# Kernel tuning notes

Hardware: AMD Instinct MI355X
Metric: run time of the kernel (lower is better)

Reference implementation:

```python
import jax, jax.numpy as jnp
import numpy as np

N_NODES = 98304
N_GRAPHS = 2048
NODES_PER_GRAPH = 48
N_EDGES = 393216
NODE_IN = 128
EMB = 64
HID = 256
N_LAYERS = 6
ATTN_DIM = 256
N_HEADS = 4
HEAD_DIM = ATTN_DIM // N_HEADS
OUT_DIM = 1024


def setup_inputs() -> dict:
    key = jax.random.key(0)
    ks = iter(jax.random.split(key, 40))

    def nrm(shape, fan_in):
        return (jax.random.normal(next(ks), shape, dtype=jnp.float32)
                / np.float32(np.sqrt(fan_in)))

    x = jax.random.normal(next(ks), (N_NODES, NODE_IN), dtype=jnp.float32)
    edge_index = jax.random.randint(next(ks), (2, N_EDGES), 0, N_NODES, dtype=jnp.int32)
    batch = (jnp.arange(N_NODES, dtype=jnp.int32) // NODES_PER_GRAPH)

    inp = {
        "x": x,
        "edge_index": edge_index,
        "batch": batch,
        "W_embed": nrm((NODE_IN, EMB), NODE_IN),
        "b_embed": jnp.zeros((EMB,), jnp.float32),
        "W1": nrm((N_LAYERS, EMB, HID), EMB),
        "b1": jnp.zeros((N_LAYERS, HID), jnp.float32),
        "W2": nrm((N_LAYERS, HID, 2 * HID), HID),
        "b2": jnp.zeros((N_LAYERS, 2 * HID), jnp.float32),
        "W3": nrm((N_LAYERS, 2 * HID, EMB), 2 * HID),
        "b3": jnp.zeros((N_LAYERS, EMB), jnp.float32),
        "Wp": nrm((EMB, ATTN_DIM), EMB),
        "bp": jnp.zeros((ATTN_DIM,), jnp.float32),
        "q": jax.random.normal(next(ks), (1, ATTN_DIM), dtype=jnp.float32),
        "W_in": nrm((ATTN_DIM, 3 * ATTN_DIM), ATTN_DIM),
        "b_in": jnp.zeros((3 * ATTN_DIM,), jnp.float32),
        "W_out": nrm((ATTN_DIM, ATTN_DIM), ATTN_DIM),
        "b_out": jnp.zeros((ATTN_DIM,), jnp.float32),
        "Wh1": nrm((ATTN_DIM, HID), ATTN_DIM),
        "bh1": jnp.zeros((HID,), jnp.float32),
        "ln_g": jnp.ones((HID,), jnp.float32),
        "ln_b": jnp.zeros((HID,), jnp.float32),
        "Wh2": nrm((HID, OUT_DIM), HID),
        "bh2": jnp.zeros((OUT_DIM,), jnp.float32),
    }
    return inp


def _forward(x, edge_index, batch, W_embed, b_embed, W1, b1, W2, b2, W3, b3,
             Wp, bp, q, W_in, b_in, W_out, b_out, Wh1, bh1, ln_g, ln_b, Wh2, bh2):
    row = edge_index[0]  # only row is used, matching the torch module

    # node embed
    h = x @ W_embed + b_embed  # [N, 64]

    # 6 GNN layers: gather h[row] -> 3-layer MLP -> scatter_add back to row
    for l in range(N_LAYERS):
        m = jax.nn.relu(h[row] @ W1[l] + b1[l])          # [E, 256]
        m = jax.nn.relu(m @ W2[l] + b2[l])               # [E, 512]
        dh = m @ W3[l] + b3[l]                           # [E, 64]
        h = h + jax.ops.segment_sum(dh, row, num_segments=N_NODES)

    # attention pooling per graph (single learned query, 4 heads)
    hp = h @ Wp + bp                                     # [N, 256]
    Wq, Wk, Wv = W_in[:, :ATTN_DIM], W_in[:, ATTN_DIM:2 * ATTN_DIM], W_in[:, 2 * ATTN_DIM:]
    bq, bk, bv = b_in[:ATTN_DIM], b_in[ATTN_DIM:2 * ATTN_DIM], b_in[2 * ATTN_DIM:]

    qh = ((q @ Wq + bq).reshape(N_HEADS, HEAD_DIM)
          / jnp.asarray(np.sqrt(HEAD_DIM), jnp.float32))  # [H, D]
    k = (hp @ Wk + bk).reshape(N_NODES, N_HEADS, HEAD_DIM)
    v = (hp @ Wv + bv).reshape(N_NODES, N_HEADS, HEAD_DIM)

    scores = jnp.einsum('nhd,hd->nh', k, qh)             # [N, H]
    smax = jax.ops.segment_max(scores, batch, num_segments=N_GRAPHS)  # [B, H]
    e = jnp.exp(scores - smax[batch])
    denom = jax.ops.segment_sum(e, batch, num_segments=N_GRAPHS)      # [B, H]
    w = e / denom[batch]                                  # [N, H]
    pooled = jax.ops.segment_sum(w[:, :, None] * v, batch, num_segments=N_GRAPHS)  # [B, H, D]
    attn = pooled.reshape(N_GRAPHS, ATTN_DIM) @ W_out + b_out  # [B, 256]

    # projection head: ReLU -> Linear -> ReLU -> LayerNorm -> Linear
    t = jax.nn.relu(attn) @ Wh1 + bh1
    t = jax.nn.relu(t)
    mu = jnp.mean(t, axis=-1, keepdims=True)
    var = jnp.mean((t - mu) ** 2, axis=-1, keepdims=True)
    t = (t - mu) * jax.lax.rsqrt(var + 1e-5) * ln_g + ln_b
    return t @ Wh2 + bh2                                  # [B, 1024]


def reference(x, edge_index, batch, W_embed, b_embed, W1, b1, W2, b2, W3, b3,
              Wp, bp, q, W_in, b_in, W_out, b_out, Wh1, bh1, ln_g, ln_b, Wh2, bh2):
    return _forward(x, edge_index, batch, W_embed, b_embed, W1, b1, W2, b2, W3, b3,
                    Wp, bp, q, W_in, b_in, W_out, b_out, Wh1, bh1, ln_g, ln_b, Wh2, bh2)
```

## Files before the change

### kernel.cpp

```cpp
#include <hip/hip_runtime.h>
#include <hip/hip_bf16.h>

#define N_NODES 98304
#define N_GRAPHS 2048
#define N_EDGES 393216
#define EMB 64
#define HID 256
#define N_LAYERS_ 6

typedef __attribute__((ext_vector_type(8))) short short8v;
typedef __attribute__((ext_vector_type(4))) float f32x4;
typedef __attribute__((ext_vector_type(16))) float f32x16;
#define MFMA16(a, b, c) __builtin_amdgcn_mfma_f32_16x16x32_bf16(a, b, c, 0, 0, 0)
#define MFMA32(a, b, c) __builtin_amdgcn_mfma_f32_32x32x16_bf16(a, b, c, 0, 0, 0)

__device__ __forceinline__ unsigned short f2bf(float x) {
    unsigned int u = __float_as_uint(x);
    u = (u + 0x7fffu + ((u >> 16) & 1u)) >> 16;
    return (unsigned short)u;
}
__device__ __forceinline__ float bf2f(unsigned short h) {
    return __uint_as_float(((unsigned int)h) << 16);
}
__device__ __forceinline__ unsigned int cvtpk(float a, float b) {
    unsigned int r;
    asm("v_cvt_pk_bf16_f32 %0, %1, %2" : "=v"(r) : "v"(a), "v"(b));
    return r;
}
__device__ __forceinline__ int swz(int row, int col, int rowc) {
    return (row * rowc + col) ^ ((row & ((rowc >> 3) - 1)) << 3);
}

__global__ __launch_bounds__(256) void zero_cnt_kernel(int* __restrict__ cnt) {
    int i = blockIdx.x * 256 + threadIdx.x;
    if (i < N_NODES) cnt[i] = 0;
}
__global__ __launch_bounds__(256) void hist_kernel(const int* __restrict__ row,
                                                   int* __restrict__ cnt) {
    int i = blockIdx.x * 256 + threadIdx.x;
    if (i < N_EDGES) atomicAdd(&cnt[row[i]], 1);
}

__global__ __launch_bounds__(64) void prep_frag_kernel(
    const float* __restrict__ W, unsigned short* __restrict__ oh,
    unsigned short* __restrict__ ol, int K, int N)
{
    const int NF = N >> 4, KS = K >> 5;
    const int fpl = NF * KS;
    const int layer = blockIdx.x / fpl;
    const int fid = blockIdx.x % fpl;
    const int nf = fid / KS, ks = fid % KS;
    const int lane = threadIdx.x;
    const float* Wl = W + (size_t)layer * K * N;
    const int n = nf * 16 + (lane & 15);
    const int kb = ks * 32 + (lane >> 4) * 8;
    short8v vh, vl;
    #pragma unroll
    for (int j = 0; j < 8; j++) {
        float wv = Wl[(size_t)(kb + j) * N + n];
        unsigned short hi = f2bf(wv);
        vh[j] = (short)hi;
        vl[j] = (short)f2bf(wv - bf2f(hi));
    }
    size_t o = (size_t)layer * K * N + ((size_t)(nf * KS + ks) * 64 + lane) * 8;
    *reinterpret_cast<short8v*>(oh + o) = vh;
    *reinterpret_cast<short8v*>(ol + o) = vl;
}

__global__ __launch_bounds__(64) void prep_frag32_kernel(
    const float* __restrict__ W, unsigned short* __restrict__ oh,
    unsigned short* __restrict__ ol, int K, int N)
{
    const int NF = N >> 5, KS = K >> 4;
    const int fpl = NF * KS;
    const int layer = blockIdx.x / fpl;
    const int fid = blockIdx.x % fpl;
    const int nf = fid / KS, ks = fid % KS;
    const int lane = threadIdx.x;
    const float* Wl = W + (size_t)layer * K * N;
    const int n = nf * 32 + (lane & 31);
    const int kb = ks * 16 + (lane >> 5) * 8;
    short8v vh, vl;
    #pragma unroll
    for (int j = 0; j < 8; j++) {
        float wv = Wl[(size_t)(kb + j) * N + n];
        unsigned short hi = f2bf(wv);
        vh[j] = (short)hi;
        vl[j] = (short)f2bf(wv - bf2f(hi));
    }
    size_t o = (size_t)layer * K * N + ((size_t)(nf * KS + ks) * 64 + lane) * 8;
    *reinterpret_cast<short8v*>(oh + o) = vh;
    *reinterpret_cast<short8v*>(ol + o) = vl;
}

__global__ __launch_bounds__(256) void gbuild_kernel(
    const float* __restrict__ Wp, const float* __restrict__ bp,
    const float* __restrict__ W_in, const float* __restrict__ b_in,
    float* __restrict__ Gm, float* __restrict__ Gd)
{
    const int idx = blockIdx.x * 256 + threadIdx.x;
    const int q = idx >> 8, p = idx & 255;
    float s = 0.f;
    if ((q >> 6) == (p >> 6)) {
        const float* wr = Wp + (q & 63) * 256;
        for (int j = 0; j < 256; j++) s += wr[j] * W_in[j * 768 + 512 + p];
    }
    Gm[q * 256 + p] = s;
    if (blockIdx.x == 0) {
        const int pp = threadIdx.x;
        float dsum = b_in[512 + pp];
        for (int j = 0; j < 256; j++) dsum += bp[j] * W_in[j * 768 + 512 + pp];
        Gd[pp] = dsum;
    }
}

__global__ __launch_bounds__(256) void embed_mfma_kernel(
    const float* __restrict__ x,
    const unsigned short* __restrict__ Weh, const unsigned short* __restrict__ Wel,
    const float* __restrict__ b, float* __restrict__ h)
{
    __shared__ __attribute__((aligned(16))) unsigned short xh[32 * 128];
    __shared__ __attribute__((aligned(16))) unsigned short xl[32 * 128];
    const int tid = threadIdx.x;
    const int lane = tid & 63, w = tid >> 6;
    const int lm = lane & 15, lq = lane >> 4;
    const int base = blockIdx.x * 32;
    {
        int row = tid >> 3, c0 = (tid & 7) * 16;
        const float4* p = reinterpret_cast<const float4*>(x + (size_t)(base + row) * 128 + c0);
        #pragma unroll
        for (int g = 0; g < 4; g++) {
            float4 u = p[g];
            unsigned int p01 = cvtpk(u.x, u.y);
            unsigned int p23 = cvtpk(u.z, u.w);
            float h0 = __uint_as_float(p01 << 16), h1 = __uint_as_float(p01 & 0xffff0000u);
            float h2 = __uint_as_float(p23 << 16), h3 = __uint_as_float(p23 & 0xffff0000u);
            unsigned int q01 = cvtpk(u.x - h0, u.y - h1);
            unsigned int q23 = cvtpk(u.z - h2, u.w - h3);
            int idx = swz(row, c0 + g * 4, 128);
            *reinterpret_cast<uint2*>(&xh[idx]) = make_uint2(p01, p23);
            *reinterpret_cast<uint2*>(&xl[idx]) = make_uint2(q01, q23);
        }
    }
    __syncthreads();
    f32x4 acc0, acc1;
    {
        float bv = b[w * 16 + lm];
        acc0 = f32x4{bv, bv, bv, bv};
        acc1 = acc0;
    }
    #pragma unroll
    for (int ks = 0; ks < 4; ks++) {
        short8v a0h = *reinterpret_cast<const short8v*>(&xh[swz(lm, ks * 32 + lq * 8, 128)]);
        short8v a0l = *reinterpret_cast<const short8v*>(&xl[swz(lm, ks * 32 + lq * 8, 128)]);
        short8v a1h = *reinterpret_cast<const short8v*>(&xh[swz(16 + lm, ks * 32 + lq * 8, 128)]);
        short8v a1l = *reinterpret_cast<const short8v*>(&xl[swz(16 + lm, ks * 32 + lq * 8, 128)]);
        size_t bi = ((size_t)(w * 4 + ks) * 64 + lane) * 8;
        short8v bh = *reinterpret_cast<const short8v*>(Weh + bi);
        short8v bl = *reinterpret_cast<const short8v*>(Wel + bi);
        acc0 = MFMA16(a0h, bh, acc0); acc0 = MFMA16(a0l, bh, acc0); acc0 = MFMA16(a0h, bl, acc0);
        acc1 = MFMA16(a1h, bh, acc1); acc1 = MFMA16(a1l, bh, acc1); acc1 = MFMA16(a1h, bl, acc1);
    }
    #pragma unroll
    for (int r = 0; r < 4; r++) {
        h[(size_t)(base + lq * 4 + r) * 64 + w * 16 + lm] = acc0[r];
        h[(size_t)(base + 16 + lq * 4 + r) * 64 + w * 16 + lm] = acc1[r];
    }
}

__device__ __forceinline__ void store_quad(
    unsigned short* __restrict__ oh, unsigned short* __restrict__ ol,
    float v0, float v1, float v2, float v3,
    int row0, int col, int rowc)
{
    unsigned int p01 = cvtpk(v0, v1);
    unsigned int p23 = cvtpk(v2, v3);
    float h0 = __uint_as_float(p01 << 16), h1 = __uint_as_float(p01 & 0xffff0000u);
    float h2 = __uint_as_float(p23 << 16), h3 = __uint_as_float(p23 & 0xffff0000u);
    unsigned int q01 = cvtpk(v0 - h0, v1 - h1);
    unsigned int q23 = cvtpk(v2 - h2, v3 - h3);
    oh[swz(row0 + 0, col, rowc)] = (unsigned short)p01;
    oh[swz(row0 + 1, col, rowc)] = (unsigned short)(p01 >> 16);
    oh[swz(row0 + 2, col, rowc)] = (unsigned short)p23;
    oh[swz(row0 + 3, col, rowc)] = (unsigned short)(p23 >> 16);
    ol[swz(row0 + 0, col, rowc)] = (unsigned short)q01;
    ol[swz(row0 + 1, col, rowc)] = (unsigned short)(q01 >> 16);
    ol[swz(row0 + 2, col, rowc)] = (unsigned short)q23;
    ol[swz(row0 + 3, col, rowc)] = (unsigned short)(q23 >> 16);
}

__global__ __launch_bounds__(512, 4) void layer_mfma_kernel(
    float* __restrict__ h, const int* __restrict__ cnt,
    const unsigned short* __restrict__ W1h, const unsigned short* __restrict__ W1l,
    const float* __restrict__ b1,
    const unsigned short* __restrict__ W2h, const unsigned short* __restrict__ W2l,
    const float* __restrict__ b2,
    const unsigned short* __restrict__ W3h, const unsigned short* __restrict__ W3l,
    const float* __restrict__ b3)
{
    __shared__ __attribute__((aligned(16))) unsigned short m1_[16384];
    __shared__ __attribute__((aligned(16))) unsigned short m2_[16384];
    unsigned short* m1h_ = m1_;
    unsigned short* m1l_ = m1_ + 8192;
    unsigned short* m2h_ = m2_;
    unsigned short* m2l_ = m2_ + 8192;
    unsigned short* hsh = m2_;
    unsigned short* hsl = m2_ + 2048;
    float* scr = reinterpret_cast<float*>(m1_);

    const int tid = threadIdx.x;
    const int lane = tid & 63, w = tid >> 6;
    const int lr = lane & 31, lh = lane >> 5;
    const int base = blockIdx.x * 32;

    {
        int row = tid >> 4, c0 = (tid & 15) * 4;
        const float4 u = *reinterpret_cast<const float4*>(h + (size_t)(base + row) * 64 + c0);
        unsigned int p01 = cvtpk(u.x, u.y);
        unsigned int p23 = cvtpk(u.z, u.w);
        float h0 = __uint_as_float(p01 << 16), h1 = __uint_as_float(p01 & 0xffff0000u);
        float h2 = __uint_as_float(p23 << 16), h3 = __uint_as_float(p23 & 0xffff0000u);
        unsigned int q01 = cvtpk(u.x - h0, u.y - h1);
        unsigned int q23 = cvtpk(u.z - h2, u.w - h3);
        int idx = swz(row, c0, 64);
        *reinterpret_cast<uint2*>(&hsh[idx]) = make_uint2(p01, p23);
        *reinterpret_cast<uint2*>(&hsl[idx]) = make_uint2(q01, q23);
    }
    __syncthreads();

    {
        f32x16 a0, a1;
        float bv = b1[w * 32 + lr];
        #pragma unroll
        for (int i = 0; i < 16; i++) { a0[i] = bv; a1[i] = 0.f; }
        #pragma unroll
        for (int ks = 0; ks < 4; ks++) {
            short8v ah = *reinterpret_cast<const short8v*>(&hsh[swz(lr, ks * 16 + lh * 8, 64)]);
            short8v al = *reinterpret_cast<const short8v*>(&hsl[swz(lr, ks * 16 + lh * 8, 64)]);
            size_t bi = ((size_t)(w * 4 + ks) * 64 + lane) * 8;
            short8v bh = *reinterpret_cast<const short8v*>(W1h + bi);
            short8v bl = *reinterpret_cast<const short8v*>(W1l + bi);
            if (ks & 1) {
                a1 = MFMA32(ah, bh, a1); a1 = MFMA32(al, bh, a1); a1 = MFMA32(ah, bl, a1);
            } else {
                a0 = MFMA32(ah, bh, a0); a0 = MFMA32(al, bh, a0); a0 = MFMA32(ah, bl, a0);
            }
        }
        #pragma unroll
        for (int q = 0; q < 4; q++)
            store_quad(m1h_, m1l_,
                fmaxf(a0[4 * q + 0] + a1[4 * q + 0], 0.f),
                fmaxf(a0[4 * q + 1] + a1[4 * q + 1], 0.f),
                fmaxf(a0[4 * q + 2] + a1[4 * q + 2], 0.f),
                fmaxf(a0[4 * q + 3] + a1[4 * q + 3], 0.f),
                8 * q + 4 * lh, w * 32 + lr, 256);
    }
    __syncthreads();

    const int nfc = w & 1, kq = w >> 1;
    f32x16 d0, d1;
    {
        float bv = (kq == 0) ? b3[nfc * 32 + lr] : 0.f;
        #pragma unroll
        for (int i = 0; i < 16; i++) { d0[i] = bv; d1[i] = 0.f; }
    }

    #pragma unroll
    for (int c = 0; c < 2; ++c) {
        {
            const int nf = c * 8 + w;
            f32x16 a0, a1;
            float bv = b2[nf * 32 + lr];
            #pragma unroll
            for (int i = 0; i < 16; i++) { a0[i] = bv; a1[i] = 0.f; }
            #pragma unroll
            for (int kk = 0; kk < 16; kk++) {
                short8v ah = *reinterpret_cast<const short8v*>(&m1h_[swz(lr, kk * 16 + lh * 8, 256)]);
                short8v al = *reinterpret_cast<const short8v*>(&m1l_[swz(lr, kk * 16 + lh * 8, 256)]);
                size_t bi = ((size_t)(nf * 16 + kk) * 64 + lane) * 8;
                short8v bh = *reinterpret_cast<const short8v*>(W2h + bi);
                short8v bl = *reinterpret_cast<const short8v*>(W2l + bi);
                if (kk & 1) {
                    a1 = MFMA32(ah, bh, a1); a1 = MFMA32(al, bh, a1); a1 = MFMA32(ah, bl, a1);
                } else {
                    a0 = MFMA32(ah, bh, a0); a0 = MFMA32(al, bh, a0); a0 = MFMA32(ah, bl, a0);
                }
            }
            __syncthreads();
            #pragma unroll
            for (int q = 0; q < 4; q++)
                store_quad(m2h_, m2l_,
                    fmaxf(a0[4 * q + 0] + a1[4 * q + 0], 0.f),
                    fmaxf(a0[4 * q + 1] + a1[4 * q + 1], 0.f),
                    fmaxf(a0[4 * q + 2] + a1[4 * q + 2], 0.f),
                    fmaxf(a0[4 * q + 3] + a1[4 * q + 3], 0.f),
                    8 * q + 4 * lh, w * 32 + lr, 256);
        }
        __syncthreads();
        #pragma unroll
        for (int kk = 0; kk < 4; kk++) {
            int kg = kq * 4 + kk;
            short8v ah = *reinterpret_cast<const short8v*>(&m2h_[swz(lr, kg * 16 + lh * 8, 256)]);
            short8v al = *reinterpret_cast<const short8v*>(&m2l_[swz(lr, kg * 16 + lh * 8, 256)]);
            size_t bi = ((size_t)(nfc * 32 + c * 16 + kg) * 64 + lane) * 8;
            short8v bh = *reinterpret_cast<const short8v*>(W3h + bi);
            short8v bl = *reinterpret_cast<const short8v*>(W3l + bi);
            if (kk & 1) {
                d1 = MFMA32(ah, bh, d1); d1 = MFMA32(al, bh, d1); d1 = MFMA32(ah, bl, d1);
            } else {
                d0 = MFMA32(ah, bh, d0); d0 = MFMA32(al, bh, d0); d0 = MFMA32(ah, bl, d0);
            }
        }
    }
    __syncthreads();

    {
        f32x16 dv = d0 + d1;
        #pragma unroll
        for (int q = 0; q < 4; q++)
            #pragma unroll
            for (int r = 0; r < 4; r++) {
                int row = 8 * q + 4 * lh + r;
                scr[kq * 2048 + row * 64 + nfc * 32 + lr] = dv[4 * q + r];
            }
    }
    __syncthreads();
    {
        int i0 = tid * 4;
        int row = i0 >> 6, col = i0 & 63;
        int rr = base + row;
        float cv = (float)cnt[rr];
        f32x4 s0 = *reinterpret_cast<f32x4*>(&scr[i0]);
        f32x4 s1 = *reinterpret_cast<f32x4*>(&scr[2048 + i0]);
        f32x4 s2 = *reinterpret_cast<f32x4*>(&scr[4096 + i0]);
        f32x4 s3 = *reinterpret_cast<f32x4*>(&scr[6144 + i0]);
        float4* hp = reinterpret_cast<float4*>(h + (size_t)rr * 64 + col);
        float4 hv = *hp;
        hv.x += cv * (s0[0] + s1[0] + s2[0] + s3[0]);
        hv.y += cv * (s0[1] + s1[1] + s2[1] + s3[1]);
        hv.z += cv * (s0[2] + s1[2] + s2[2] + s3[2]);
        hv.w += cv * (s0[3] + s1[3] + s2[3] + s3[3]);
        *hp = hv;
    }
}

__global__ __launch_bounds__(256) void prec_kernel(
    const float* __restrict__ q, const float* __restrict__ W_in,
    const float* __restrict__ b_in, const float* __restrict__ Wp,
    const float* __restrict__ bp, float* __restrict__ prec)
{
    __shared__ float qh_s[256];
    __shared__ float u_s[4 * 256];
    const int tid = threadIdx.x;
    {
        float acc = b_in[tid];
        for (int j = 0; j < 256; j++) acc += q[j] * W_in[j * 768 + tid];
        qh_s[tid] = acc * 0.125f;
    }
    __syncthreads();
    {
        #pragma unroll
        for (int hd = 0; hd < 4; hd++) {
            float a = 0.f;
            for (int d = 0; d < 64; d++)
                a += W_in[tid * 768 + 256 + hd * 64 + d] * qh_s[hd * 64 + d];
            u_s[hd * 256 + tid] = a;
        }
    }
    __syncthreads();
    {
        int hd = tid >> 6, i = tid & 63;
        float a = 0.f;
        for (int j = 0; j < 256; j++) a += Wp[i * 256 + j] * u_s[hd * 256 + j];
        prec[hd * 64 + i] = a;
    }
    if (tid < 4) {
        float a = 0.f;
        for (int j = 0; j < 256; j++) a += bp[j] * u_s[tid * 256 + j];
        for (int d = 0; d < 64; d++) a += b_in[256 + tid * 64 + d] * qh_s[tid * 64 + d];
        prec[256 + tid] = a;
    }
}

__global__ __launch_bounds__(64) void attnpool_kernel(
    const float* __restrict__ h, const float* __restrict__ prec,
    float* __restrict__ hw)
{
    __shared__ float hs[48 * 65];
    __shared__ float ss[4 * 64];
    __shared__ float ds_[4];
    __shared__ float wl[48 * 4];
    const int lane = threadIdx.x;
    const int g = blockIdx.x;
    #pragma unroll
    for (int hd = 0; hd < 4; hd++) ss[hd * 64 + lane] = prec[hd * 64 + lane];
    if (lane < 4) ds_[lane] = prec[256 + lane];
    for (int r = 0; r < 48; r++)
        hs[r * 65 + lane] = h[((size_t)g * 48 + r) * 64 + lane];
    __syncthreads();
    float sc[4] = {0.f, 0.f, 0.f, 0.f};
    if (lane < 48) {
        #pragma unroll
        for (int hd = 0; hd < 4; hd++) sc[hd] = ds_[hd];
        for (int c = 0; c < 64; c++) {
            float a = hs[lane * 65 + c];
            #pragma unroll
            for (int hd = 0; hd < 4; hd++) sc[hd] += a * ss[hd * 64 + c];
        }
    }
    #pragma unroll
    for (int hd = 0; hd < 4; hd++) {
        float v = (lane < 48) ? sc[hd] : -3.0e38f;
        #pragma unroll
        for (int m = 32; m >= 1; m >>= 1) v = fmaxf(v, __shfl_xor(v, m, 64));
        float e = (lane < 48) ? __expf(sc[hd] - v) : 0.f;
        float s = e;
        #pragma unroll
        for (int m = 32; m >= 1; m >>= 1) s += __shfl_xor(s, m, 64);
        if (lane < 48) wl[lane * 4 + hd] = e / s;
    }
    __syncthreads();
    float acc[4] = {0.f, 0.f, 0.f, 0.f};
    for (int n = 0; n < 48; n++) {
        float hv = hs[n * 65 + lane];
        #pragma unroll
        for (int hd = 0; hd < 4; hd++) acc[hd] += wl[n * 4 + hd] * hv;
    }
    #pragma unroll
    for (int hd = 0; hd < 4; hd++) hw[(size_t)g * 256 + hd * 64 + lane] = acc[hd];
}

__device__ __forceinline__ void tail_stage(
    const unsigned short* __restrict__ inh, const unsigned short* __restrict__ inl,
    const unsigned short* __restrict__ wh, const unsigned short* __restrict__ wl,
    const float* __restrict__ bias, const bool do_relu,
    unsigned short* __restrict__ oth, unsigned short* __restrict__ otl,
    float* __restrict__ tf32,
    const int w, const int lane, const int lm, const int lq)
{
    f32x4 acc[2][2];
    #pragma unroll
    for (int f = 0; f < 2; f++) {
        float bv = bias[(2 * w + f) * 16 + lm];
        acc[f][0] = f32x4{bv, bv, bv, bv};
        acc[f][1] = acc[f][0];
    }
    #pragma unroll
    for (int ks = 0; ks < 8; ks++) {
        short8v ah0 = *reinterpret_cast<const short8v*>(&inh[swz(lm, ks * 32 + lq * 8, 256)]);
        short8v al0 = *reinterpret_cast<const short8v*>(&inl[swz(lm, ks * 32 + lq * 8, 256)]);
        short8v ah1 = *reinterpret_cast<const short8v*>(&inh[swz(16 + lm, ks * 32 + lq * 8, 256)]);
        short8v al1 = *reinterpret_cast<const short8v*>(&inl[swz(16 + lm, ks * 32 + lq * 8, 256)]);
        #pragma unroll
        for (int f = 0; f < 2; f++) {
            size_t bi = ((size_t)((2 * w + f) * 8 + ks) * 64 + lane) * 8;
            short8v bh = *reinterpret_cast<const short8v*>(wh + bi);
            short8v bl = *reinterpret_cast<const short8v*>(wl + bi);
            acc[f][0] = MFMA16(ah0, bh, acc[f][0]);
            acc[f][0] = MFMA16(al0, bh, acc[f][0]);
            acc[f][0] = MFMA16(ah0, bl, acc[f][0]);
            acc[f][1] = MFMA16(ah1, bh, acc[f][1]);
            acc[f][1] = MFMA16(al1, bh, acc[f][1]);
            acc[f][1] = MFMA16(ah1, bl, acc[f][1]);
        }
    }
    #pragma unroll
    for (int f = 0; f < 2; f++)
        #pragma unroll
        for (int m = 0; m < 2; m++) {
            if (tf32) {
                #pragma unroll
                for (int r = 0; r < 4; r++) {
                    float v = acc[f][m][r];
                    if (do_relu) v = fmaxf(v, 0.f);
                    tf32[(m * 16 + lq * 4 + r) * 256 + (2 * w + f) * 16 + lm] = v;
                }
            } else {
                float v0 = acc[f][m][0], v1 = acc[f][m][1], v2 = acc[f][m][2], v3 = acc[f][m][3];
                if (do_relu) {
                    v0 = fmaxf(v0, 0.f); v1 = fmaxf(v1, 0.f);
                    v2 = fmaxf(v2, 0.f); v3 = fmaxf(v3, 0.f);
                }
                store_quad(oth, otl, v0, v1, v2, v3,
                           m * 16 + lq * 4, (2 * w + f) * 16 + lm, 256);
            }
        }
}

__global__ __launch_bounds__(512, 4) void tail_mfma_kernel(
    const float* __restrict__ hw,
    const unsigned short* __restrict__ Gh, const unsigned short* __restrict__ Gl,
    const float* __restrict__ Gd,
    const unsigned short* __restrict__ Woh, const unsigned short* __restrict__ Wol,
    const float* __restrict__ b_out,
    const unsigned short* __restrict__ Wh1h, const unsigned short* __restrict__ Wh1l,
    const float* __restrict__ bh1,
    const float* __restrict__ ln_g, const float* __restrict__ ln_b,
    const unsigned short* __restrict__ Wh2h, const unsigned short* __restrict__ Wh2l,
    const float* __restrict__ bh2,
    float* __restrict__ out)
{
    __shared__ __attribute__((aligned(16))) unsigned short L[32768];
    unsigned short* Ah = L;
    unsigned short* Al = L + 8192;
    unsigned short* Bh = L + 16384;
    unsigned short* Bl = L + 24576;
    float* tf = reinterpret_cast<float*>(L + 16384);
    const int tid = threadIdx.x;
    const int lane = tid & 63, w = tid >> 6;
    const int lm = lane & 15, lq = lane >> 4;
    const int g0 = blockIdx.x * 32;

    {
        const float4* hp = reinterpret_cast<const float4*>(hw + (size_t)g0 * 256);
        #pragma unroll
        for (int i = 0; i < 4; i++) {
            int e = tid + 512 * i;
            int row = e >> 6, c0 = (e & 63) * 4;
            float4 u = hp[e];
            unsigned int p01 = cvtpk(u.x, u.y);
            unsigned int p23 = cvtpk(u.z, u.w);
            float h0 = __uint_as_float(p01 << 16), h1 = __uint_as_float(p01 & 0xffff0000u);
            float h2 = __uint_as_float(p23 << 16), h3 = __uint_as_float(p23 & 0xffff0000u);
            unsigned int q01 = cvtpk(u.x - h0, u.y - h1);
            unsigned int q23 = cvtpk(u.z - h2, u.w - h3);
            int idx = swz(row, c0, 256);
            *reinterpret_cast<uint2*>(&Ah[idx]) = make_uint2(p01, p23);
            *reinterpret_cast<uint2*>(&Al[idx]) = make_uint2(q01, q23);
        }
    }
    __syncthreads();
    tail_stage(Ah, Al, Gh, Gl, Gd, false, Bh, Bl, nullptr, w, lane, lm, lq);
    __syncthreads();
    tail_stage(Bh, Bl, Woh, Wol, b_out, true, Ah, Al, nullptr, w, lane, lm, lq);
    __syncthreads();
    tail_stage(Ah, Al, Wh1h, Wh1l, bh1, true, nullptr, nullptr, tf, w, lane, lm, lq);
    __syncthreads();
    {
        const int row = tid >> 4, l16 = tid & 15;
        float s = 0.f;
        #pragma unroll
        for (int k = 0; k < 16; k++) s += tf[row * 256 + l16 + 16 * k];
        #pragma unroll
        for (int m = 1; m < 16; m <<= 1) s += __shfl_xor(s, m, 16);
        float mu = s * (1.f / 256.f);
        float v = 0.f;
        #pragma unroll
        for (int k = 0; k < 16; k++) {
            float d = tf[row * 256 + l16 + 16 * k] - mu;
            v += d * d;
        }
        #pragma unroll
        for (int m = 1; m < 16; m <<= 1) v += __shfl_xor(v, m, 16);
        float rs = rsqrtf(v * (1.f / 256.f) + 1e-5f);
        #pragma unroll
        for (int k = 0; k < 16; k++) {
            int col = l16 + 16 * k;
            float val = (tf[row * 256 + col] - mu) * rs * ln_g[col] + ln_b[col];
            unsigned short hi = f2bf(val);
            int idx = swz(row, col, 256);
            Ah[idx] = hi;
            Al[idx] = f2bf(val - bf2f(hi));
        }
    }
    __syncthreads();
    {
        f32x4 acc[8][2];
        #pragma unroll
        for (int f = 0; f < 8; f++) {
            float bv = bh2[(8 * w + f) * 16 + lm];
            acc[f][0] = f32x4{bv, bv, bv, bv};
            acc[f][1] = acc[f][0];
        }
        #pragma unroll
        for (int ks = 0; ks < 8; ks++) {
            short8v ah0 = *reinterpret_cast<const short8v*>(&Ah[swz(lm, ks * 32 + lq * 8, 256)]);
            short8v al0 = *reinterpret_cast<const short8v*>(&Al[swz(lm, ks * 32 + lq * 8, 256)]);
            short8v ah1 = *reinterpret_cast<const short8v*>(&Ah[swz(16 + lm, ks * 32 + lq * 8, 256)]);
            short8v al1 = *reinterpret_cast<const short8v*>(&Al[swz(16 + lm, ks * 32 + lq * 8, 256)]);
            #pragma unroll
            for (int f = 0; f < 8; f++) {
                size_t bi = ((size_t)((8 * w + f) * 8 + ks) * 64 + lane) * 8;
                short8v bh = *reinterpret_cast<const short8v*>(Wh2h + bi);
                short8v bl = *reinterpret_cast<const short8v*>(Wh2l + bi);
                acc[f][0] = MFMA16(ah0, bh, acc[f][0]);
                acc[f][0] = MFMA16(al0, bh, acc[f][0]);
                acc[f][0] = MFMA16(ah0, bl, acc[f][0]);
                acc[f][1] = MFMA16(ah1, bh, acc[f][1]);
                acc[f][1] = MFMA16(al1, bh, acc[f][1]);
                acc[f][1] = MFMA16(ah1, bl, acc[f][1]);
            }
        }
        #pragma unroll
        for (int f = 0; f < 8; f++)
            #pragma unroll
            for (int m = 0; m < 2; m++)
                #pragma unroll
                for (int r = 0; r < 4; r++)
                    out[(size_t)(g0 + m * 16 + lq * 4 + r) * 1024 + (8 * w + f) * 16 + lm]
                        = acc[f][m][r];
    }
}

extern "C" void kernel_launch(void* const* d_in, const int* in_sizes, int n_in,
                              void* d_out, int out_size, void* d_ws, size_t ws_size,
                              hipStream_t stream) {
    const float* x       = (const float*)d_in[0];
    const int*   edge    = (const int*)d_in[1];
    const float* W_embed = (const float*)d_in[3];
    const float* b_embed = (const float*)d_in[4];
    const float* W1 = (const float*)d_in[5];
    const float* b1 = (const float*)d_in[6];
    const float* W2 = (const float*)d_in[7];
    const float* b2 = (const float*)d_in[8];
    const float* W3 = (const float*)d_in[9];
    const float* b3 = (const float*)d_in[10];
    const float* Wp = (const float*)d_in[11];
    const float* bp = (const float*)d_in[12];
    const float* q  = (const float*)d_in[13];
    const float* W_in  = (const float*)d_in[14];
    const float* b_in  = (const float*)d_in[15];
    const float* W_out = (const float*)d_in[16];
    const float* b_out = (const float*)d_in[17];
    const float* Wh1 = (const float*)d_in[18];
    const float* bh1 = (const float*)d_in[19];
    const float* ln_g = (const float*)d_in[20];
    const float* ln_b = (const float*)d_in[21];
    const float* Wh2 = (const float*)d_in[22];
    const float* bh2 = (const float*)d_in[23];
    float* out = (float*)d_out;

    char* ws = (char*)d_ws;
    int*   cnt  = (int*)(ws + 0);
    float* h    = (float*)(ws + 393216);
    float* hw   = (float*)(ws + 25559040);
    float* prec = (float*)(ws + 27656192);
    unsigned short* W1h = (unsigned short*)(ws + 27657232);
    unsigned short* W1l = (unsigned short*)(ws + 27853840);
    unsigned short* W2h = (unsigned short*)(ws + 28050448);
    unsigned short* W2l = (unsigned short*)(ws + 29623312);
    unsigned short* W3h = (unsigned short*)(ws + 31196176);
    unsigned short* W3l = (unsigned short*)(ws + 31589392);
    unsigned short* Weh = (unsigned short*)(ws + 31982608);
    unsigned short* Wel = (unsigned short*)(ws + 31998992);
    float* Gm  = (float*)(ws + 32015376);
    float* Gd  = (float*)(ws + 32277520);
    unsigned short* Gfh  = (unsigned short*)(ws + 32278544);
    unsigned short* Gfl  = (unsigned short*)(ws + 32409616);
    unsigned short* Wofh = (unsigned short*)(ws + 32540688);
    unsigned short* Wofl = (unsigned short*)(ws + 32671760);
    unsigned short* Wh1fh= (unsigned short*)(ws + 32802832);
    unsigned short* Wh1fl= (unsigned short*)(ws + 32933904);
    unsigned short* Wh2fh= (unsigned short*)(ws + 33064976);
    unsigned short* Wh2fl= (unsigned short*)(ws + 33589264);

    zero_cnt_kernel<<<N_NODES / 256, 256, 0, stream>>>(cnt);
    hist_kernel<<<N_EDGES / 256, 256, 0, stream>>>(edge, cnt);

    prep_frag_kernel<<<1 * (64 / 16) * (128 / 32), 64, 0, stream>>>(W_embed, Weh, Wel, 128, 64);
    prep_frag32_kernel<<<6 * (256 / 32) * (64 / 16), 64, 0, stream>>>(W1, W1h, W1l, 64, 256);
    prep_frag32_kernel<<<6 * (512 / 32) * (256 / 16), 64, 0, stream>>>(W2, W2h, W2l, 256, 512);
    prep_frag32_kernel<<<6 * (64 / 32) * (512 / 16), 64, 0, stream>>>(W3, W3h, W3l, 512, 64);

    gbuild_kernel<<<256, 256, 0, stream>>>(Wp, bp, W_in, b_in, Gm, Gd);
    prep_frag_kernel<<<(256 / 16) * (256 / 32), 64, 0, stream>>>(Gm, Gfh, Gfl, 256, 256);
    prep_frag_kernel<<<(256 / 16) * (256 / 32), 64, 0, stream>>>(W_out, Wofh, Wofl, 256, 256);
    prep_frag_kernel<<<(256 / 16) * (256 / 32), 64, 0, stream>>>(Wh1, Wh1fh, Wh1fl, 256, 256);
    prep_frag_kernel<<<(1024 / 16) * (256 / 32), 64, 0, stream>>>(Wh2, Wh2fh, Wh2fl, 256, 1024);

    embed_mfma_kernel<<<N_NODES / 32, 256, 0, stream>>>(x, Weh, Wel, b_embed, h);
    for (int l = 0; l < N_LAYERS_; l++) {
        layer_mfma_kernel<<<N_NODES / 32, 512, 0, stream>>>(
            h, cnt,
            W1h + (size_t)l * EMB * HID,     W1l + (size_t)l * EMB * HID,     b1 + (size_t)l * HID,
            W2h + (size_t)l * HID * 2 * HID, W2l + (size_t)l * HID * 2 * HID, b2 + (size_t)l * 2 * HID,
            W3h + (size_t)l * 2 * HID * EMB, W3l + (size_t)l * 2 * HID * EMB, b3 + (size_t)l * EMB);
    }
    prec_kernel<<<1, 256, 0, stream>>>(q, W_in, b_in, Wp, bp, prec);
    attnpool_kernel<<<N_GRAPHS, 64, 0, stream>>>(h, prec, hw);
    tail_mfma_kernel<<<N_GRAPHS / 32, 512, 0, stream>>>(
        hw, Gfh, Gfl, Gd, Wofh, Wofl, b_out, Wh1fh, Wh1fl, bh1,
        ln_g, ln_b, Wh2fh, Wh2fl, bh2, out);
}
```

Baseline: 895.8 us.

## Process 64 nodes per block in layer MLP to reuse weight fragments

The per-layer MLP kernel now handles 64 node rows per block instead of 32. Each wave computes two 32-row M tiles against the same weight fragment loaded from global memory, which halves weight traffic per node. Shared memory per block doubles, the launch bound's minimum occupancy drops from 4 to 2 blocks, and register pressure rises from the doubled accumulators. One barrier before the scratch write is removed, and a barrier is added after the first MLP stage so that m1 writes do not overlap the aliased input-staging area.

```diff
diff --git a/kernel.cpp b/kernel.cpp
--- a/kernel.cpp
+++ b/kernel.cpp
@@ -189,7 +189,7 @@
     ol[swz(row0 + 3, col, rowc)] = (unsigned short)(q23 >> 16);
 }
 
-__global__ __launch_bounds__(512, 4) void layer_mfma_kernel(
+__global__ __launch_bounds__(512, 2) void layer_mfma_kernel(
     float* __restrict__ h, const int* __restrict__ cnt,
     const unsigned short* __restrict__ W1h, const unsigned short* __restrict__ W1l,
     const float* __restrict__ b1,
@@ -198,149 +198,189 @@
     const unsigned short* __restrict__ W3h, const unsigned short* __restrict__ W3l,
     const float* __restrict__ b3)
 {
-    __shared__ __attribute__((aligned(16))) unsigned short m1_[16384];
-    __shared__ __attribute__((aligned(16))) unsigned short m2_[16384];
+    __shared__ __attribute__((aligned(16))) unsigned short m1_[32768];
+    __shared__ __attribute__((aligned(16))) unsigned short m2_[32768];
     unsigned short* m1h_ = m1_;
-    unsigned short* m1l_ = m1_ + 8192;
+    unsigned short* m1l_ = m1_ + 16384;
     unsigned short* m2h_ = m2_;
-    unsigned short* m2l_ = m2_ + 8192;
+    unsigned short* m2l_ = m2_ + 16384;
     unsigned short* hsh = m2_;
-    unsigned short* hsl = m2_ + 2048;
+    unsigned short* hsl = m2_ + 4096;
     float* scr = reinterpret_cast<float*>(m1_);
 
     const int tid = threadIdx.x;
     const int lane = tid & 63, w = tid >> 6;
     const int lr = lane & 31, lh = lane >> 5;
-    const int base = blockIdx.x * 32;
-
-    {
-        int row = tid >> 4, c0 = (tid & 15) * 4;
-        const float4 u = *reinterpret_cast<const float4*>(h + (size_t)(base + row) * 64 + c0);
-        unsigned int p01 = cvtpk(u.x, u.y);
-        unsigned int p23 = cvtpk(u.z, u.w);
-        float h0 = __uint_as_float(p01 << 16), h1 = __uint_as_float(p01 & 0xffff0000u);
-        float h2 = __uint_as_float(p23 << 16), h3 = __uint_as_float(p23 & 0xffff0000u);
-        unsigned int q01 = cvtpk(u.x - h0, u.y - h1);
-        unsigned int q23 = cvtpk(u.z - h2, u.w - h3);
-        int idx = swz(row, c0, 64);
-        *reinterpret_cast<uint2*>(&hsh[idx]) = make_uint2(p01, p23);
-        *reinterpret_cast<uint2*>(&hsl[idx]) = make_uint2(q01, q23);
-    }
-    __syncthreads();
-
-    {
-        f32x16 a0, a1;
+    const int base = blockIdx.x * 64;
+
+    {
+        int row = tid >> 3, c0 = (tid & 7) * 8;
+        const float4* p = reinterpret_cast<const float4*>(h + (size_t)(base + row) * 64 + c0);
+        #pragma unroll
+        for (int g = 0; g < 2; g++) {
+            float4 u = p[g];
+            unsigned int p01 = cvtpk(u.x, u.y);
+            unsigned int p23 = cvtpk(u.z, u.w);
+            float h0 = __uint_as_float(p01 << 16), h1 = __uint_as_float(p01 & 0xffff0000u);
+            float h2 = __uint_as_float(p23 << 16), h3 = __uint_as_float(p23 & 0xffff0000u);
+            unsigned int q01 = cvtpk(u.x - h0, u.y - h1);
+            unsigned int q23 = cvtpk(u.z - h2, u.w - h3);
+            int idx = swz(row, c0 + g * 4, 64);
+            *reinterpret_cast<uint2*>(&hsh[idx]) = make_uint2(p01, p23);
+            *reinterpret_cast<uint2*>(&hsl[idx]) = make_uint2(q01, q23);
+        }
+    }
+    __syncthreads();
+
+    {
+        f32x16 a0m0, a1m0, a0m1, a1m1;
         float bv = b1[w * 32 + lr];
         #pragma unroll
-        for (int i = 0; i < 16; i++) { a0[i] = bv; a1[i] = 0.f; }
+        for (int i = 0; i < 16; i++) {
+            a0m0[i] = bv; a1m0[i] = 0.f; a0m1[i] = bv; a1m1[i] = 0.f;
+        }
         #pragma unroll
         for (int ks = 0; ks < 4; ks++) {
-            short8v ah = *reinterpret_cast<const short8v*>(&hsh[swz(lr, ks * 16 + lh * 8, 64)]);
-            short8v al = *reinterpret_cast<const short8v*>(&hsl[swz(lr, ks * 16 + lh * 8, 64)]);
+            short8v ah0 = *reinterpret_cast<const short8v*>(&hsh[swz(lr, ks * 16 + lh * 8, 64)]);
+            short8v al0 = *reinterpret_cast<const short8v*>(&hsl[swz(lr, ks * 16 + lh * 8, 64)]);
+            short8v ah1 = *reinterpret_cast<const short8v*>(&hsh[swz(32 + lr, ks * 16 + lh * 8, 64)]);
+            short8v al1 = *reinterpret_cast<const short8v*>(&hsl[swz(32 + lr, ks * 16 + lh * 8, 64)]);
             size_t bi = ((size_t)(w * 4 + ks) * 64 + lane) * 8;
             short8v bh = *reinterpret_cast<const short8v*>(W1h + bi);
             short8v bl = *reinterpret_cast<const short8v*>(W1l + bi);
             if (ks & 1) {
-                a1 = MFMA32(ah, bh, a1); a1 = MFMA32(al, bh, a1); a1 = MFMA32(ah, bl, a1);
+                a1m0 = MFMA32(ah0, bh, a1m0); a1m0 = MFMA32(al0, bh, a1m0); a1m0 = MFMA32(ah0, bl, a1m0);
+                a1m1 = MFMA32(ah1, bh, a1m1); a1m1 = MFMA32(al1, bh, a1m1); a1m1 = MFMA32(ah1, bl, a1m1);
             } else {
-                a0 = MFMA32(ah, bh, a0); a0 = MFMA32(al, bh, a0); a0 = MFMA32(ah, bl, a0);
+                a0m0 = MFMA32(ah0, bh, a0m0); a0m0 = MFMA32(al0, bh, a0m0); a0m0 = MFMA32(ah0, bl, a0m0);
+                a0m1 = MFMA32(ah1, bh, a0m1); a0m1 = MFMA32(al1, bh, a0m1); a0m1 = MFMA32(ah1, bl, a0m1);
             }
         }
-        #pragma unroll
-        for (int q = 0; q < 4; q++)
+        __syncthreads();
+        #pragma unroll
+        for (int q = 0; q < 4; q++) {
             store_quad(m1h_, m1l_,
-                fmaxf(a0[4 * q + 0] + a1[4 * q + 0], 0.f),
-                fmaxf(a0[4 * q + 1] + a1[4 * q + 1], 0.f),
-                fmaxf(a0[4 * q + 2] + a1[4 * q + 2], 0.f),
-                fmaxf(a0[4 * q + 3] + a1[4 * q + 3], 0.f),
+                fmaxf(a0m0[4 * q + 0] + a1m0[4 * q + 0], 0.f),
+                fmaxf(a0m0[4 * q + 1] + a1m0[4 * q + 1], 0.f),
+                fmaxf(a0m0[4 * q + 2] + a1m0[4 * q + 2], 0.f),
+                fmaxf(a0m0[4 * q + 3] + a1m0[4 * q + 3], 0.f),
                 8 * q + 4 * lh, w * 32 + lr, 256);
+            store_quad(m1h_, m1l_,
+                fmaxf(a0m1[4 * q + 0] + a1m1[4 * q + 0], 0.f),
+                fmaxf(a0m1[4 * q + 1] + a1m1[4 * q + 1], 0.f),
+                fmaxf(a0m1[4 * q + 2] + a1m1[4 * q + 2], 0.f),
+                fmaxf(a0m1[4 * q + 3] + a1m1[4 * q + 3], 0.f),
+                32 + 8 * q + 4 * lh, w * 32 + lr, 256);
+        }
     }
     __syncthreads();
 
     const int nfc = w & 1, kq = w >> 1;
-    f32x16 d0, d1;
+    f32x16 d0m0, d1m0, d0m1, d1m1;
     {
         float bv = (kq == 0) ? b3[nfc * 32 + lr] : 0.f;
         #pragma unroll
-        for (int i = 0; i < 16; i++) { d0[i] = bv; d1[i] = 0.f; }
+        for (int i = 0; i < 16; i++) {
+            d0m0[i] = bv; d1m0[i] = 0.f; d0m1[i] = bv; d1m1[i] = 0.f;
+        }
     }
 
     #pragma unroll
     for (int c = 0; c < 2; ++c) {
         {
             const int nf = c * 8 + w;
-            f32x16 a0, a1;
+            f32x16 b0m0, b1m0, b0m1, b1m1;
             float bv = b2[nf * 32 + lr];
             #pragma unroll
-            for (int i = 0; i < 16; i++) { a0[i] = bv; a1[i] = 0.f; }
+            for (int i = 0; i < 16; i++) {
+                b0m0[i] = bv; b1m0[i] = 0.f; b0m1[i] = bv; b1m1[i] = 0.f;
+            }
             #pragma unroll
             for (int kk = 0; kk < 16; kk++) {
-                short8v ah = *reinterpret_cast<const short8v*>(&m1h_[swz(lr, kk * 16 + lh * 8, 256)]);
-                short8v al = *reinterpret_cast<const short8v*>(&m1l_[swz(lr, kk * 16 + lh * 8, 256)]);
+                short8v ah0 = *reinterpret_cast<const short8v*>(&m1h_[swz(lr, kk * 16 + lh * 8, 256)]);
+                short8v al0 = *reinterpret_cast<const short8v*>(&m1l_[swz(lr, kk * 16 + lh * 8, 256)]);
+                short8v ah1 = *reinterpret_cast<const short8v*>(&m1h_[swz(32 + lr, kk * 16 + lh * 8, 256)]);
+                short8v al1 = *reinterpret_cast<const short8v*>(&m1l_[swz(32 + lr, kk * 16 + lh * 8, 256)]);
                 size_t bi = ((size_t)(nf * 16 + kk) * 64 + lane) * 8;
                 short8v bh = *reinterpret_cast<const short8v*>(W2h + bi);
                 short8v bl = *reinterpret_cast<const short8v*>(W2l + bi);
                 if (kk & 1) {
-                    a1 = MFMA32(ah, bh, a1); a1 = MFMA32(al, bh, a1); a1 = MFMA32(ah, bl, a1);
+                    b1m0 = MFMA32(ah0, bh, b1m0); b1m0 = MFMA32(al0, bh, b1m0); b1m0 = MFMA32(ah0, bl, b1m0);
+                    b1m1 = MFMA32(ah1, bh, b1m1); b1m1 = MFMA32(al1, bh, b1m1); b1m1 = MFMA32(ah1, bl, b1m1);
                 } else {
-                    a0 = MFMA32(ah, bh, a0); a0 = MFMA32(al, bh, a0); a0 = MFMA32(ah, bl, a0);
+                    b0m0 = MFMA32(ah0, bh, b0m0); b0m0 = MFMA32(al0, bh, b0m0); b0m0 = MFMA32(ah0, bl, b0m0);
+                    b0m1 = MFMA32(ah1, bh, b0m1); b0m1 = MFMA32(al1, bh, b0m1); b0m1 = MFMA32(ah1, bl, b0m1);
                 }
             }
             __syncthreads();
             #pragma unroll
-            for (int q = 0; q < 4; q++)
+            for (int q = 0; q < 4; q++) {
                 store_quad(m2h_, m2l_,
-                    fmaxf(a0[4 * q + 0] + a1[4 * q + 0], 0.f),
-                    fmaxf(a0[4 * q + 1] + a1[4 * q + 1], 0.f),
-                    fmaxf(a0[4 * q + 2] + a1[4 * q + 2], 0.f),
-                    fmaxf(a0[4 * q + 3] + a1[4 * q + 3], 0.f),
+                    fmaxf(b0m0[4 * q + 0] + b1m0[4 * q + 0], 0.f),
+                    fmaxf(b0m0[4 * q + 1] + b1m0[4 * q + 1], 0.f),
+                    fmaxf(b0m0[4 * q + 2] + b1m0[4 * q + 2], 0.f),
+                    fmaxf(b0m0[4 * q + 3] + b1m0[4 * q + 3], 0.f),
                     8 * q + 4 * lh, w * 32 + lr, 256);
+                store_quad(m2h_, m2l_,
+                    fmaxf(b0m1[4 * q + 0] + b1m1[4 * q + 0], 0.f),
+                    fmaxf(b0m1[4 * q + 1] + b1m1[4 * q + 1], 0.f),
+                    fmaxf(b0m1[4 * q + 2] + b1m1[4 * q + 2], 0.f),
+                    fmaxf(b0m1[4 * q + 3] + b1m1[4 * q + 3], 0.f),
+                    32 + 8 * q + 4 * lh, w * 32 + lr, 256);
+            }
         }
         __syncthreads();
         #pragma unroll
         for (int kk = 0; kk < 4; kk++) {
             int kg = kq * 4 + kk;
-            short8v ah = *reinterpret_cast<const short8v*>(&m2h_[swz(lr, kg * 16 + lh * 8, 256)]);
-            short8v al = *reinterpret_cast<const short8v*>(&m2l_[swz(lr, kg * 16 + lh * 8, 256)]);
+            short8v ah0 = *reinterpret_cast<const short8v*>(&m2h_[swz(lr, kg * 16 + lh * 8, 256)]);
+            short8v al0 = *reinterpret_cast<const short8v*>(&m2l_[swz(lr, kg * 16 + lh * 8, 256)]);
+            short8v ah1 = *reinterpret_cast<const short8v*>(&m2h_[swz(32 + lr, kg * 16 + lh * 8, 256)]);
+            short8v al1 = *reinterpret_cast<const short8v*>(&m2l_[swz(32 + lr, kg * 16 + lh * 8, 256)]);
             size_t bi = ((size_t)(nfc * 32 + c * 16 + kg) * 64 + lane) * 8;
             short8v bh = *reinterpret_cast<const short8v*>(W3h + bi);
             short8v bl = *reinterpret_cast<const short8v*>(W3l + bi);
             if (kk & 1) {
-                d1 = MFMA32(ah, bh, d1); d1 = MFMA32(al, bh, d1); d1 = MFMA32(ah, bl, d1);
+                d1m0 = MFMA32(ah0, bh, d1m0); d1m0 = MFMA32(al0, bh, d1m0); d1m0 = MFMA32(ah0, bl, d1m0);
+                d1m1 = MFMA32(ah1, bh, d1m1); d1m1 = MFMA32(al1, bh, d1m1); d1m1 = MFMA32(ah1, bl, d1m1);
             } else {
-                d0 = MFMA32(ah, bh, d0); d0 = MFMA32(al, bh, d0); d0 = MFMA32(ah, bl, d0);
+                d0m0 = MFMA32(ah0, bh, d0m0); d0m0 = MFMA32(al0, bh, d0m0); d0m0 = MFMA32(ah0, bl, d0m0);
+                d0m1 = MFMA32(ah1, bh, d0m1); d0m1 = MFMA32(al1, bh, d0m1); d0m1 = MFMA32(ah1, bl, d0m1);
             }
         }
     }
-    __syncthreads();
-
-    {
-        f32x16 dv = d0 + d1;
+    {
+        f32x16 dv0 = d0m0 + d1m0;
+        f32x16 dv1 = d0m1 + d1m1;
         #pragma unroll
         for (int q = 0; q < 4; q++)
             #pragma unroll
             for (int r = 0; r < 4; r++) {
                 int row = 8 * q + 4 * lh + r;
-                scr[kq * 2048 + row * 64 + nfc * 32 + lr] = dv[4 * q + r];
+                scr[kq * 4096 + row * 64 + nfc * 32 + lr] = dv0[4 * q + r];
+                scr[kq * 4096 + (32 + row) * 64 + nfc * 32 + lr] = dv1[4 * q + r];
             }
     }
     __syncthreads();
     {
-        int i0 = tid * 4;
-        int row = i0 >> 6, col = i0 & 63;
+        int row = tid >> 3, c0 = (tid & 7) * 8;
         int rr = base + row;
         float cv = (float)cnt[rr];
-        f32x4 s0 = *reinterpret_cast<f32x4*>(&scr[i0]);
-        f32x4 s1 = *reinterpret_cast<f32x4*>(&scr[2048 + i0]);
-        f32x4 s2 = *reinterpret_cast<f32x4*>(&scr[4096 + i0]);
-        f32x4 s3 = *reinterpret_cast<f32x4*>(&scr[6144 + i0]);
-        float4* hp = reinterpret_cast<float4*>(h + (size_t)rr * 64 + col);
-        float4 hv = *hp;
-        hv.x += cv * (s0[0] + s1[0] + s2[0] + s3[0]);
-        hv.y += cv * (s0[1] + s1[1] + s2[1] + s3[1]);
-        hv.z += cv * (s0[2] + s1[2] + s2[2] + s3[2]);
-        hv.w += cv * (s0[3] + s1[3] + s2[3] + s3[3]);
-        *hp = hv;
+        float4* hp = reinterpret_cast<float4*>(h + (size_t)rr * 64 + c0);
+        #pragma unroll
+        for (int g = 0; g < 2; g++) {
+            int i0 = row * 64 + c0 + g * 4;
+            f32x4 s0 = *reinterpret_cast<f32x4*>(&scr[i0]);
+            f32x4 s1 = *reinterpret_cast<f32x4*>(&scr[4096 + i0]);
+            f32x4 s2 = *reinterpret_cast<f32x4*>(&scr[8192 + i0]);
+            f32x4 s3 = *reinterpret_cast<f32x4*>(&scr[12288 + i0]);
+            float4 hv = hp[g];
+            hv.x += cv * (s0[0] + s1[0] + s2[0] + s3[0]);
+            hv.y += cv * (s0[1] + s1[1] + s2[1] + s3[1]);
+            hv.z += cv * (s0[2] + s1[2] + s2[2] + s3[2]);
+            hv.w += cv * (s0[3] + s1[3] + s2[3] + s3[3]);
+            hp[g] = hv;
+        }
     }
 }
 
@@ -670,7 +710,7 @@
 
     embed_mfma_kernel<<<N_NODES / 32, 256, 0, stream>>>(x, Weh, Wel, b_embed, h);
     for (int l = 0; l < N_LAYERS_; l++) {
-        layer_mfma_kernel<<<N_NODES / 32, 512, 0, stream>>>(
+        layer_mfma_kernel<<<N_NODES / 64, 512, 0, stream>>>(
             h, cnt,
             W1h + (size_t)l * EMB * HID,     W1l + (size_t)l * EMB * HID,     b1 + (size_t)l * HID,
             W2h + (size_t)l * HID * 2 * HID, W2l + (size_t)l * HID * 2 * HID, b2 + (size_t)l * 2 * HID,
```

After: 889.5 us. About the same (-0.7%).
